# Kernel optimization log

Measured on AMD Instinct MI355X. Metric: run time of the kernel, lower is better.

The kernel has to match this reference:

```python
import jax, jax.numpy as jnp
import numpy as np

B = 65536      # batch of (state, action) pairs
DIM_S = 64     # input feature dim
DIM_C = 8      # number of options / experts
H = 256        # hidden width (two hidden layers)


def setup_inputs() -> dict:
    key = jax.random.key(0)
    ks = jax.random.split(key, 7)
    s = 0.05  # small init scale
    st = jax.random.normal(ks[0], (B, DIM_S), dtype=jnp.float32)
    # Batched expert weights: one slice per expert (dim_c experts).
    W1 = jax.random.normal(ks[1], (DIM_C, DIM_S, H), dtype=jnp.float32) * s
    b1 = jax.random.normal(ks[2], (DIM_C, H), dtype=jnp.float32) * s
    W2 = jax.random.normal(ks[3], (DIM_C, H, H), dtype=jnp.float32) * s
    b2 = jax.random.normal(ks[4], (DIM_C, H), dtype=jnp.float32) * s
    W3 = jax.random.normal(ks[5], (DIM_C, H, 1), dtype=jnp.float32) * s
    b3 = jax.random.normal(ks[6], (DIM_C, 1), dtype=jnp.float32) * s
    return {"st": st, "W1": W1, "b1": b1, "W2": W2, "b2": b2,
            "W3": W3, "b3": b3}


def reference(st, W1, b1, W2, b2, W3, b3):
    # Equivalent of torch.stack([m(st) for m in self.discriminator], dim=1):
    # every expert MLP (dim_s -> H -> H -> 1, ReLU) applied to the same st,
    # expressed as batched GEMMs over the expert axis c.
    h = jax.nn.relu(jnp.einsum('bs,csh->bch', st, W1) + b1[None])   # [B, C, H]
    h = jax.nn.relu(jnp.einsum('bch,chk->bck', h, W2) + b2[None])   # [B, C, H]
    d = jnp.einsum('bch,cho->bco', h, W3) + b3[None]                # [B, C, 1]
    return d
```

## Files before the change

### kernel.cpp

```cpp
#include <hip/hip_runtime.h>
#include <hip/hip_bf16.h>

typedef __bf16 bf16x8 __attribute__((ext_vector_type(8)));
typedef float  f32x4  __attribute__((ext_vector_type(4)));

static constexpr int S  = 64;
static constexpr int C  = 8;
static constexpr int HD = 256;

__device__ __forceinline__ unsigned short f2bf(float f) {
  __hip_bfloat16 b = __float2bfloat16(f);
  unsigned short u;
  __builtin_memcpy(&u, &b, 2);
  return u;
}

__global__ __launch_bounds__(256) void prep_weights(
    const float* __restrict__ W1, const float* __restrict__ W2,
    unsigned short* __restrict__ W1T, unsigned short* __restrict__ W2T)
{
  int idx = blockIdx.x * 256 + threadIdx.x;
  {
    int c = idx >> 16;
    int o = idx & 65535;
    int n = o >> 8;
    int k = o & 255;
    W2T[idx] = f2bf(W2[(c << 16) + (k << 8) + n]);
  }
  if (idx < C * HD * S) {
    int c = idx >> 14;
    int o = idx & 16383;
    int h = o >> 6;
    int s = o & 63;
    W1T[idx] = f2bf(W1[(c << 14) + (s << 8) + h]);
  }
}

__global__ __launch_bounds__(256, 2) void moe_fused(
    const float* __restrict__ st,
    const unsigned short* __restrict__ W1T,
    const unsigned short* __restrict__ W2T,
    const float* __restrict__ b1,
    const float* __restrict__ b2,
    const float* __restrict__ W3,
    const float* __restrict__ b3,
    float* __restrict__ out)
{
  constexpr int LDA  = 72;
  constexpr int LDW1 = 72;
  constexpr int LDW2 = 264;

  __shared__ __align__(16) unsigned short sA[128 * LDA];
  __shared__ __align__(16) unsigned short sW[256 * LDW1];

  const int tid  = threadIdx.x;
  const int lane = tid & 63;
  const int wv   = tid >> 6;
  const int l15  = lane & 15;
  const int q    = lane >> 4;
  const int c    = blockIdx.x & 7;
  const int row0 = (blockIdx.x >> 3) * 128;

  {
    const float4* stv = reinterpret_cast<const float4*>(st + (size_t)row0 * S);
    #pragma unroll
    for (int i = 0; i < 8; ++i) {
      int f = tid + i * 256;
      int m = f >> 4;
      int qq = f & 15;
      float4 v = stv[f];
      ushort4 p;
      p.x = f2bf(v.x); p.y = f2bf(v.y); p.z = f2bf(v.z); p.w = f2bf(v.w);
      *reinterpret_cast<ushort4*>(sA + m * LDA + qq * 4) = p;
    }
    const uint4* w1v = reinterpret_cast<const uint4*>(W1T + c * HD * S);
    #pragma unroll
    for (int i = 0; i < 8; ++i) {
      int f = tid + i * 256;
      int n = f >> 3;
      int qq = f & 7;
      *reinterpret_cast<uint4*>(sW + n * LDW1 + qq * 8) = w1v[f];
    }
  }
  __syncthreads();

  bf16x8 aF[4][2][2];

  {
    f32x4 acc[2][16];
    #pragma unroll
    for (int rt = 0; rt < 2; ++rt)
      #pragma unroll
      for (int ct = 0; ct < 16; ++ct)
        acc[rt][ct] = (f32x4){0.f, 0.f, 0.f, 0.f};

    #pragma unroll
    for (int ks = 0; ks < 2; ++ks) {
      const int koff = ks * 32 + q * 8;
      bf16x8 a0 = *reinterpret_cast<const bf16x8*>(sA + (wv * 32 + l15) * LDA + koff);
      bf16x8 a1 = *reinterpret_cast<const bf16x8*>(sA + (wv * 32 + 16 + l15) * LDA + koff);
      #pragma unroll
      for (int ct = 0; ct < 16; ++ct) {
        bf16x8 b = *reinterpret_cast<const bf16x8*>(sW + (ct * 16 + l15) * LDW1 + koff);
        acc[0][ct] = __builtin_amdgcn_mfma_f32_16x16x32_bf16(a0, b, acc[0][ct], 0, 0, 0);
        acc[1][ct] = __builtin_amdgcn_mfma_f32_16x16x32_bf16(a1, b, acc[1][ct], 0, 0, 0);
      }
    }

    #pragma unroll
    for (int cc = 0; cc < 4; ++cc) {
      #pragma unroll
      for (int rt = 0; rt < 2; ++rt) {
        const int rbase = wv * 32 + rt * 16 + q * 4;
        #pragma unroll
        for (int ctl = 0; ctl < 4; ++ctl) {
          const int ct  = cc * 4 + ctl;
          const int col = ct * 16 + l15;
          const float bias = b1[c * HD + col];
          #pragma unroll
          for (int r = 0; r < 4; ++r) {
            float v = acc[rt][ct][r] + bias;
            v = v > 0.f ? v : 0.f;
            sA[(rbase + r) * LDA + ctl * 16 + l15] = f2bf(v);
          }
        }
      }
      __syncthreads();
      #pragma unroll
      for (int rt = 0; rt < 2; ++rt)
        #pragma unroll
        for (int k2 = 0; k2 < 2; ++k2)
          aF[cc][rt][k2] = *reinterpret_cast<const bf16x8*>(
              sA + (wv * 32 + rt * 16 + l15) * LDA + k2 * 32 + q * 8);
      __syncthreads();
    }
  }

  float dacc[2][4];
  #pragma unroll
  for (int rt = 0; rt < 2; ++rt)
    #pragma unroll
    for (int r = 0; r < 4; ++r) dacc[rt][r] = 0.f;

  const unsigned short* W2c = W2T + c * HD * HD;
  for (int ch = 0; ch < 4; ++ch) {
    {
      const uint4* src = reinterpret_cast<const uint4*>(W2c + ch * 64 * HD);
      #pragma unroll
      for (int i = 0; i < 8; ++i) {
        int f = tid + i * 256;
        int n = f >> 5;
        int qq = f & 31;
        *reinterpret_cast<uint4*>(sW + n * LDW2 + qq * 8) = src[f];
      }
    }
    __syncthreads();

    f32x4 acc[2][4];
    #pragma unroll
    for (int rt = 0; rt < 2; ++rt)
      #pragma unroll
      for (int ct = 0; ct < 4; ++ct)
        acc[rt][ct] = (f32x4){0.f, 0.f, 0.f, 0.f};

    #pragma unroll
    for (int ks = 0; ks < 8; ++ks) {
      const int koff = ks * 32 + q * 8;
      const int cc = ks >> 1, k2 = ks & 1;
      #pragma unroll
      for (int ct = 0; ct < 4; ++ct) {
        bf16x8 b = *reinterpret_cast<const bf16x8*>(sW + (ct * 16 + l15) * LDW2 + koff);
        acc[0][ct] = __builtin_amdgcn_mfma_f32_16x16x32_bf16(aF[cc][0][k2], b, acc[0][ct], 0, 0, 0);
        acc[1][ct] = __builtin_amdgcn_mfma_f32_16x16x32_bf16(aF[cc][1][k2], b, acc[1][ct], 0, 0, 0);
      }
    }

    #pragma unroll
    for (int ct = 0; ct < 4; ++ct) {
      const int n = ch * 64 + ct * 16 + l15;
      const float bias = b2[c * HD + n];
      const float w3v  = W3[c * HD + n];
      #pragma unroll
      for (int rt = 0; rt < 2; ++rt)
        #pragma unroll
        for (int r = 0; r < 4; ++r) {
          float v = acc[rt][ct][r] + bias;
          v = v > 0.f ? v : 0.f;
          dacc[rt][r] += v * w3v;
        }
    }
    __syncthreads();
  }

  #pragma unroll
  for (int rt = 0; rt < 2; ++rt)
    #pragma unroll
    for (int r = 0; r < 4; ++r) {
      float v = dacc[rt][r];
      v += __shfl_xor(v, 1);
      v += __shfl_xor(v, 2);
      v += __shfl_xor(v, 4);
      v += __shfl_xor(v, 8);
      dacc[rt][r] = v;
    }

  if (l15 == 0) {
    const float bb = b3[c];
    const int rbase = row0 + wv * 32 + q * 4;
    #pragma unroll
    for (int rt = 0; rt < 2; ++rt)
      #pragma unroll
      for (int r = 0; r < 4; ++r)
        out[(rbase + rt * 16 + r) * C + c] = dacc[rt][r] + bb;
  }
}

extern "C" void kernel_launch(void* const* d_in, const int* in_sizes, int n_in,
                              void* d_out, int out_size, void* d_ws, size_t ws_size,
                              hipStream_t stream)
{
  const float* st = (const float*)d_in[0];
  const float* W1 = (const float*)d_in[1];
  const float* b1 = (const float*)d_in[2];
  const float* W2 = (const float*)d_in[3];
  const float* b2 = (const float*)d_in[4];
  const float* W3 = (const float*)d_in[5];
  const float* b3 = (const float*)d_in[6];
  float* out = (float*)d_out;

  unsigned short* W1T = (unsigned short*)d_ws;
  unsigned short* W2T = W1T + C * HD * S;

  prep_weights<<<dim3(2048), dim3(256), 0, stream>>>(W1, W2, W1T, W2T);
  moe_fused<<<dim3(4096), dim3(256), 0, stream>>>(st, W1T, W2T, b1, b2, W3, b3, out);
}
```

Before: 185.1 us.

## Double-buffer W2 chunks, read W1 from global, and tile weight transpose

The weight-prep kernel now transposes through a padded shared-memory tile so both its reads and writes are coalesced, and it launches fewer blocks. The fused kernel puts the expert index in the high bits of the block id so neighbouring blocks share one expert's weights. It loads st straight into registers and reads W1 fragments directly from global memory, so layer 1 no longer stages through shared memory or needs block barriers. W2 arrives in 32-row chunks through double-buffered shared memory, with the next chunk prefetched into registers during the current MFMAs. Smaller LDS use and launch bounds of 3 aim for higher occupancy, at the cost of uncached global W1 reads and more register pressure.

Result: slower. 302.3 us (+63.3%).

```diff
diff --git a/kernel.cpp b/kernel.cpp
--- a/kernel.cpp
+++ b/kernel.cpp
@@ -19,24 +19,44 @@
     const float* __restrict__ W1, const float* __restrict__ W2,
     unsigned short* __restrict__ W1T, unsigned short* __restrict__ W2T)
 {
-  int idx = blockIdx.x * 256 + threadIdx.x;
-  {
-    int c = idx >> 16;
-    int o = idx & 65535;
-    int n = o >> 8;
-    int k = o & 255;
-    W2T[idx] = f2bf(W2[(c << 16) + (k << 8) + n]);
-  }
-  if (idx < C * HD * S) {
-    int c = idx >> 14;
-    int o = idx & 16383;
-    int h = o >> 6;
-    int s = o & 63;
-    W1T[idx] = f2bf(W1[(c << 14) + (s << 8) + h]);
-  }
-}
-
-__global__ __launch_bounds__(256, 2) void moe_fused(
+  __shared__ float tile[32][33];
+  const int tid = threadIdx.x, cl = tid & 31, r0 = tid >> 5;
+  const int b = blockIdx.x;
+  if (b < 512) {
+    const int c = b >> 6, t = b & 63, kt = t >> 3, nt = t & 7;
+    const float* src = W2 + c * 65536;
+    #pragma unroll
+    for (int i = 0; i < 4; ++i) {
+      int r = r0 + 8 * i;
+      tile[r][cl] = src[(kt * 32 + r) * 256 + nt * 32 + cl];
+    }
+    __syncthreads();
+    unsigned short* dst = W2T + c * 65536;
+    #pragma unroll
+    for (int i = 0; i < 4; ++i) {
+      int r = r0 + 8 * i;
+      dst[(nt * 32 + r) * 256 + kt * 32 + cl] = f2bf(tile[cl][r]);
+    }
+  } else {
+    const int bb = b - 512;
+    const int c = bb >> 4, t = bb & 15, st2 = t >> 3, ht = t & 7;
+    const float* src = W1 + c * 16384;
+    #pragma unroll
+    for (int i = 0; i < 4; ++i) {
+      int r = r0 + 8 * i;
+      tile[r][cl] = src[(st2 * 32 + r) * 256 + ht * 32 + cl];
+    }
+    __syncthreads();
+    unsigned short* dst = W1T + c * 16384;
+    #pragma unroll
+    for (int i = 0; i < 4; ++i) {
+      int r = r0 + 8 * i;
+      dst[(ht * 32 + r) * 64 + st2 * 32 + cl] = f2bf(tile[cl][r]);
+    }
+  }
+}
+
+__global__ __launch_bounds__(256, 3) void moe_fused(
     const float* __restrict__ st,
     const unsigned short* __restrict__ W1T,
     const unsigned short* __restrict__ W2T,
@@ -46,95 +66,97 @@
     const float* __restrict__ b3,
     float* __restrict__ out)
 {
-  constexpr int LDA  = 72;
-  constexpr int LDW1 = 72;
+  constexpr int LDT  = 72;
   constexpr int LDW2 = 264;
-
-  __shared__ __align__(16) unsigned short sA[128 * LDA];
-  __shared__ __align__(16) unsigned short sW[256 * LDW1];
+  constexpr int CH   = 32;
+
+  __shared__ __align__(16) unsigned short sT[128 * LDT];
+  __shared__ __align__(16) unsigned short sW[2][CH * LDW2];
 
   const int tid  = threadIdx.x;
   const int lane = tid & 63;
   const int wv   = tid >> 6;
   const int l15  = lane & 15;
   const int q    = lane >> 4;
-  const int c    = blockIdx.x & 7;
-  const int row0 = (blockIdx.x >> 3) * 128;
-
+  const int c    = blockIdx.x >> 9;
+  const int row0 = (blockIdx.x & 511) * 128;
+
+  const unsigned short* W1c = W1T + c * HD * S;
+  const unsigned short* W2c = W2T + c * HD * HD;
+
+  uint4 stg[4];
   {
-    const float4* stv = reinterpret_cast<const float4*>(st + (size_t)row0 * S);
-    #pragma unroll
-    for (int i = 0; i < 8; ++i) {
-      int f = tid + i * 256;
-      int m = f >> 4;
-      int qq = f & 15;
-      float4 v = stv[f];
-      ushort4 p;
-      p.x = f2bf(v.x); p.y = f2bf(v.y); p.z = f2bf(v.z); p.w = f2bf(v.w);
-      *reinterpret_cast<ushort4*>(sA + m * LDA + qq * 4) = p;
-    }
-    const uint4* w1v = reinterpret_cast<const uint4*>(W1T + c * HD * S);
-    #pragma unroll
-    for (int i = 0; i < 8; ++i) {
-      int f = tid + i * 256;
-      int n = f >> 3;
-      int qq = f & 7;
-      *reinterpret_cast<uint4*>(sW + n * LDW1 + qq * 8) = w1v[f];
-    }
-  }
-  __syncthreads();
+    const uint4* src = reinterpret_cast<const uint4*>(W2c);
+    #pragma unroll
+    for (int i = 0; i < 4; ++i) stg[i] = src[tid + i * 256];
+  }
+
+  bf16x8 aA[2][2];
+  #pragma unroll
+  for (int rt = 0; rt < 2; ++rt)
+    #pragma unroll
+    for (int ks = 0; ks < 2; ++ks) {
+      const int row = row0 + wv * 32 + rt * 16 + l15;
+      const float4* p = reinterpret_cast<const float4*>(st + (size_t)row * S + ks * 32 + q * 8);
+      float4 x = p[0], y = p[1];
+      union { bf16x8 v; unsigned short u[8]; } a;
+      a.u[0] = f2bf(x.x); a.u[1] = f2bf(x.y); a.u[2] = f2bf(x.z); a.u[3] = f2bf(x.w);
+      a.u[4] = f2bf(y.x); a.u[5] = f2bf(y.y); a.u[6] = f2bf(y.z); a.u[7] = f2bf(y.w);
+      aA[rt][ks] = a.v;
+    }
 
   bf16x8 aF[4][2][2];
-
-  {
-    f32x4 acc[2][16];
-    #pragma unroll
-    for (int rt = 0; rt < 2; ++rt)
-      #pragma unroll
-      for (int ct = 0; ct < 16; ++ct)
-        acc[rt][ct] = (f32x4){0.f, 0.f, 0.f, 0.f};
+  #pragma unroll
+  for (int cc = 0; cc < 4; ++cc) {
+    f32x4 acc[2][4];
+    #pragma unroll
+    for (int rt = 0; rt < 2; ++rt)
+      #pragma unroll
+      for (int ctl = 0; ctl < 4; ++ctl)
+        acc[rt][ctl] = (f32x4){0.f, 0.f, 0.f, 0.f};
 
     #pragma unroll
     for (int ks = 0; ks < 2; ++ks) {
       const int koff = ks * 32 + q * 8;
-      bf16x8 a0 = *reinterpret_cast<const bf16x8*>(sA + (wv * 32 + l15) * LDA + koff);
-      bf16x8 a1 = *reinterpret_cast<const bf16x8*>(sA + (wv * 32 + 16 + l15) * LDA + koff);
-      #pragma unroll
-      for (int ct = 0; ct < 16; ++ct) {
-        bf16x8 b = *reinterpret_cast<const bf16x8*>(sW + (ct * 16 + l15) * LDW1 + koff);
-        acc[0][ct] = __builtin_amdgcn_mfma_f32_16x16x32_bf16(a0, b, acc[0][ct], 0, 0, 0);
-        acc[1][ct] = __builtin_amdgcn_mfma_f32_16x16x32_bf16(a1, b, acc[1][ct], 0, 0, 0);
-      }
-    }
-
-    #pragma unroll
-    for (int cc = 0; cc < 4; ++cc) {
-      #pragma unroll
-      for (int rt = 0; rt < 2; ++rt) {
-        const int rbase = wv * 32 + rt * 16 + q * 4;
+      #pragma unroll
+      for (int ctl = 0; ctl < 4; ++ctl) {
+        const int n = (cc * 4 + ctl) * 16 + l15;
+        bf16x8 b = *reinterpret_cast<const bf16x8*>(W1c + n * S + koff);
+        acc[0][ctl] = __builtin_amdgcn_mfma_f32_16x16x32_bf16(aA[0][ks], b, acc[0][ctl], 0, 0, 0);
+        acc[1][ctl] = __builtin_amdgcn_mfma_f32_16x16x32_bf16(aA[1][ks], b, acc[1][ctl], 0, 0, 0);
+      }
+    }
+
+    #pragma unroll
+    for (int rt = 0; rt < 2; ++rt) {
+      const int rbase = wv * 32 + rt * 16 + q * 4;
+      #pragma unroll
+      for (int ctl = 0; ctl < 4; ++ctl) {
+        const float bias = b1[c * HD + (cc * 4 + ctl) * 16 + l15];
         #pragma unroll
-        for (int ctl = 0; ctl < 4; ++ctl) {
-          const int ct  = cc * 4 + ctl;
-          const int col = ct * 16 + l15;
-          const float bias = b1[c * HD + col];
-          #pragma unroll
-          for (int r = 0; r < 4; ++r) {
-            float v = acc[rt][ct][r] + bias;
-            v = v > 0.f ? v : 0.f;
-            sA[(rbase + r) * LDA + ctl * 16 + l15] = f2bf(v);
-          }
+        for (int r = 0; r < 4; ++r) {
+          float v = acc[rt][ctl][r] + bias;
+          v = v > 0.f ? v : 0.f;
+          sT[(rbase + r) * LDT + ctl * 16 + l15] = f2bf(v);
         }
       }
-      __syncthreads();
-      #pragma unroll
-      for (int rt = 0; rt < 2; ++rt)
-        #pragma unroll
-        for (int k2 = 0; k2 < 2; ++k2)
-          aF[cc][rt][k2] = *reinterpret_cast<const bf16x8*>(
-              sA + (wv * 32 + rt * 16 + l15) * LDA + k2 * 32 + q * 8);
-      __syncthreads();
-    }
-  }
+    }
+    __asm__ __volatile__("s_waitcnt lgkmcnt(0)" ::: "memory");
+    #pragma unroll
+    for (int rt = 0; rt < 2; ++rt)
+      #pragma unroll
+      for (int k2 = 0; k2 < 2; ++k2)
+        aF[cc][rt][k2] = *reinterpret_cast<const bf16x8*>(
+            sT + (wv * 32 + rt * 16 + l15) * LDT + k2 * 32 + q * 8);
+    __asm__ __volatile__("s_waitcnt lgkmcnt(0)" ::: "memory");
+  }
+
+  #pragma unroll
+  for (int i = 0; i < 4; ++i) {
+    int f = tid + i * 256;
+    *reinterpret_cast<uint4*>(&sW[0][(f >> 5) * LDW2 + (f & 31) * 8]) = stg[i];
+  }
+  __syncthreads();
 
   float dacc[2][4];
   #pragma unroll
@@ -142,25 +164,20 @@
     #pragma unroll
     for (int r = 0; r < 4; ++r) dacc[rt][r] = 0.f;
 
-  const unsigned short* W2c = W2T + c * HD * HD;
-  for (int ch = 0; ch < 4; ++ch) {
-    {
-      const uint4* src = reinterpret_cast<const uint4*>(W2c + ch * 64 * HD);
-      #pragma unroll
-      for (int i = 0; i < 8; ++i) {
-        int f = tid + i * 256;
-        int n = f >> 5;
-        int qq = f & 31;
-        *reinterpret_cast<uint4*>(sW + n * LDW2 + qq * 8) = src[f];
-      }
-    }
-    __syncthreads();
-
-    f32x4 acc[2][4];
-    #pragma unroll
-    for (int rt = 0; rt < 2; ++rt)
-      #pragma unroll
-      for (int ct = 0; ct < 4; ++ct)
+  #pragma unroll
+  for (int ch = 0; ch < 8; ++ch) {
+    if (ch < 7) {
+      const uint4* src = reinterpret_cast<const uint4*>(W2c + (ch + 1) * CH * HD);
+      #pragma unroll
+      for (int i = 0; i < 4; ++i) stg[i] = src[tid + i * 256];
+    }
+
+    const unsigned short* buf = sW[ch & 1];
+    f32x4 acc[2][2];
+    #pragma unroll
+    for (int rt = 0; rt < 2; ++rt)
+      #pragma unroll
+      for (int ct = 0; ct < 2; ++ct)
         acc[rt][ct] = (f32x4){0.f, 0.f, 0.f, 0.f};
 
     #pragma unroll
@@ -168,16 +185,16 @@
       const int koff = ks * 32 + q * 8;
       const int cc = ks >> 1, k2 = ks & 1;
       #pragma unroll
-      for (int ct = 0; ct < 4; ++ct) {
-        bf16x8 b = *reinterpret_cast<const bf16x8*>(sW + (ct * 16 + l15) * LDW2 + koff);
+      for (int ct = 0; ct < 2; ++ct) {
+        bf16x8 b = *reinterpret_cast<const bf16x8*>(buf + (ct * 16 + l15) * LDW2 + koff);
         acc[0][ct] = __builtin_amdgcn_mfma_f32_16x16x32_bf16(aF[cc][0][k2], b, acc[0][ct], 0, 0, 0);
         acc[1][ct] = __builtin_amdgcn_mfma_f32_16x16x32_bf16(aF[cc][1][k2], b, acc[1][ct], 0, 0, 0);
       }
     }
 
     #pragma unroll
-    for (int ct = 0; ct < 4; ++ct) {
-      const int n = ch * 64 + ct * 16 + l15;
+    for (int ct = 0; ct < 2; ++ct) {
+      const int n = ch * CH + ct * 16 + l15;
       const float bias = b2[c * HD + n];
       const float w3v  = W3[c * HD + n];
       #pragma unroll
@@ -188,6 +205,14 @@
           v = v > 0.f ? v : 0.f;
           dacc[rt][r] += v * w3v;
         }
+    }
+
+    if (ch < 7) {
+      #pragma unroll
+      for (int i = 0; i < 4; ++i) {
+        int f = tid + i * 256;
+        *reinterpret_cast<uint4*>(&sW[(ch + 1) & 1][(f >> 5) * LDW2 + (f & 31) * 8]) = stg[i];
+      }
     }
     __syncthreads();
   }
@@ -231,6 +256,6 @@
   unsigned short* W1T = (unsigned short*)d_ws;
   unsigned short* W2T = W1T + C * HD * S;
 
-  prep_weights<<<dim3(2048), dim3(256), 0, stream>>>(W1, W2, W1T, W2T);
+  prep_weights<<<dim3(640), dim3(256), 0, stream>>>(W1, W2, W1T, W2T);
   moe_fused<<<dim3(4096), dim3(256), 0, stream>>>(st, W1T, W2T, b1, b2, W3, b3, out);
 }
```
